# Performance work log

Hardware: AMD Instinct MI355X
Metric: run time of the kernel (lower is better)

Reference implementation:

```python
import jax, jax.numpy as jnp
import numpy as np

INPUT_SIZE, HIDDEN_SIZE, MEMORY_SIZE, SEQ_LEN, THETA = 512, 1024, 256, 4096, 4096.0
BATCH = 8


def _expm(M):
    # scaling-and-squaring Taylor expm (float64), replaces scipy cont2discrete's expm
    nrm = np.linalg.norm(M, 1)
    s = max(0, int(np.ceil(np.log2(max(nrm, 1.0)))) + 4)
    A = M / (2.0 ** s)
    E = np.eye(M.shape[0])
    T = np.eye(M.shape[0])
    for k in range(1, 24):
        T = T @ A / k
        E = E + T
    for _ in range(s):
        E = E @ E
    return E


def _lmu_H():
    # continuous-time Legendre state-space matrices
    Q = np.arange(MEMORY_SIZE, dtype=np.float64).reshape(-1, 1)
    R = (2.0 * Q + 1.0) / THETA
    i, j = np.meshgrid(Q.ravel(), Q.ravel(), indexing="ij")
    A = R * np.where(i < j, -1.0, (-1.0) ** (i - j + 1))
    B = R * (-1.0) ** Q
    # zero-order-hold discretization with dt=1: expm([[A,B],[0,0]])
    aug = np.zeros((MEMORY_SIZE + 1, MEMORY_SIZE + 1))
    aug[:MEMORY_SIZE, :MEMORY_SIZE] = A
    aug[:MEMORY_SIZE, MEMORY_SIZE:] = B
    Md = _expm(aug)
    Ad = Md[:MEMORY_SIZE, :MEMORY_SIZE].astype(np.float32)
    Bd = Md[:MEMORY_SIZE, MEMORY_SIZE:].astype(np.float32)
    # impulse response: H[:, t] = Ad^t @ Bd  (matches torch impulse() in float32)
    H = np.empty((MEMORY_SIZE, SEQ_LEN), dtype=np.float32)
    h = Bd[:, 0]
    for t in range(SEQ_LEN):
        H[:, t] = h
        h = Ad @ h
    return H


def setup_inputs():
    key = jax.random.key(0)
    k1, k2, k3, k4, k5 = jax.random.split(key, 5)
    x = jax.random.normal(k1, (BATCH, SEQ_LEN, INPUT_SIZE), jnp.float32)
    W_u_w = jax.random.normal(k2, (1, INPUT_SIZE), jnp.float32) / np.float32(np.sqrt(INPUT_SIZE))
    W_u_b = jax.random.normal(k3, (1,), jnp.float32) * 0.01
    W_h_w = jax.random.normal(k4, (HIDDEN_SIZE, MEMORY_SIZE + INPUT_SIZE), jnp.float32) / np.float32(np.sqrt(MEMORY_SIZE + INPUT_SIZE))
    W_h_b = jax.random.normal(k5, (HIDDEN_SIZE,), jnp.float32) * 0.01
    H = jnp.asarray(_lmu_H())
    return {"x": x, "W_u_w": W_u_w, "W_u_b": W_u_b, "W_h_w": W_h_w, "W_h_b": W_h_b, "H": H}


def reference(x, W_u_w, W_u_b, W_h_w, W_h_b, H):
    B, S, D = x.shape
    # u_t = relu(W_u x_t)  -> [B, S, 1]
    u = jax.nn.relu(jnp.einsum("bsd,od->bso", x, W_u_w) + W_u_b)
    # FFT long convolution of u with impulse response H (linear conv via 2S padding)
    fft_u = jnp.fft.rfft(u.transpose(0, 2, 1), n=2 * S, axis=-1)  # [B, 1, S+1]
    fft_H = jnp.fft.rfft(H, n=2 * S, axis=-1)                     # [M, S+1]
    m = jnp.fft.irfft(fft_u * fft_H[None], n=2 * S, axis=-1)[:, :, :S]  # [B, M, S]
    m = m.transpose(0, 2, 1)                                      # [B, S, M]
    # h_t = relu(W_h [m_t; x_t])
    h = jax.nn.relu(jnp.einsum("bsk,hk->bsh", jnp.concatenate([m, x], axis=-1), W_h_w) + W_h_b)
    return h, h[:, -1, :]
```

## Files before the change

kernel.cpp:

```cpp
#include <hip/hip_runtime.h>

typedef _Float16 half8 __attribute__((ext_vector_type(8)));
typedef float f32x4 __attribute__((ext_vector_type(4)));

#define SEQ   4096
#define DIN   512
#define HID   1024
#define KMEM  256
#define NB    8
#define KC    768
#define VP    4352
#define OUT_H_ELEMS 33554432ull

__device__ __forceinline__ void load_lds16(const void* g, void* l) {
  __builtin_amdgcn_global_load_lds(
      (const __attribute__((address_space(1))) unsigned int*)g,
      (__attribute__((address_space(3))) unsigned int*)l, 16, 0, 0);
}

__global__ __launch_bounds__(256) void prep_kernel(
    const float* __restrict__ Hf, const float* __restrict__ Wf,
    _Float16* __restrict__ Hh, _Float16* __restrict__ Wh,
    _Float16* __restrict__ v2)
{
  int tid = blockIdx.x * 256 + threadIdx.x;
  int stride = gridDim.x * 256;
  for (int i = tid; i < KMEM * SEQ; i += stride) Hh[i] = (_Float16)Hf[i];
  for (int i = tid; i < HID * KC;  i += stride) Wh[i] = (_Float16)Wf[i];
  for (int i = tid; i < NB * 8 * VP; i += stride) v2[i] = (_Float16)0.f;
}

__global__ __launch_bounds__(256) void u_kernel(
    const float* __restrict__ x, const float* __restrict__ Wu,
    const float* __restrict__ Wub,
    _Float16* __restrict__ xh, _Float16* __restrict__ v2)
{
  int w = threadIdx.x >> 6, lane = threadIdx.x & 63;
  int row = blockIdx.x * 4 + w;
  const float4* xr = (const float4*)(x + (size_t)row * DIN);
  const float4* wr = (const float4*)Wu;
  float4 a0 = xr[lane * 2], a1 = xr[lane * 2 + 1];
  float4 w0 = wr[lane * 2], w1 = wr[lane * 2 + 1];
  float dot = a0.x * w0.x + a0.y * w0.y + a0.z * w0.z + a0.w * w0.w
            + a1.x * w1.x + a1.y * w1.y + a1.z * w1.z + a1.w * w1.w;
  half8 hv;
  hv[0] = (_Float16)a0.x; hv[1] = (_Float16)a0.y;
  hv[2] = (_Float16)a0.z; hv[3] = (_Float16)a0.w;
  hv[4] = (_Float16)a1.x; hv[5] = (_Float16)a1.y;
  hv[6] = (_Float16)a1.z; hv[7] = (_Float16)a1.w;
  *((half8*)(xh + (size_t)row * DIN + lane * 8)) = hv;
  #pragma unroll
  for (int off = 32; off > 0; off >>= 1) dot += __shfl_xor(dot, off);
  float u = dot + Wub[0];
  u = u > 0.f ? u : 0.f;
  if (lane < 8) {
    int s = row & (SEQ - 1), b = row >> 12;
    v2[(size_t)b * 8 * VP + (size_t)lane * VP + (4095 - s + lane)] = (_Float16)u;
  }
}

__global__ __launch_bounds__(256) void conv_kernel(
    const _Float16* __restrict__ Hh, const _Float16* __restrict__ v2,
    _Float16* __restrict__ mh)
{
  __shared__ _Float16 Bs[128 * 32];
  __shared__ _Float16 Aw[8 * 168];
  int cb = blockIdx.x;
  int b = cb >> 1, kt = cb & 1;
  int by = blockIdx.y;
  int its = (by < 16) ? (31 - by) : (by - 16);
  int s0 = its * 128, k0 = kt * 128;
  int tid = threadIdx.x;
  int w = tid >> 6, lane = tid & 63;
  int wr = w >> 1, wc = w & 1;
  int lm = lane & 15, q = lane >> 4;
  const _Float16* v2b = v2 + (size_t)b * 8 * VP;
  int gbase0 = 3968 - s0;

  const _Float16* aoff[4];
  #pragma unroll
  for (int mi = 0; mi < 4; mi++) {
    int X = wr * 64 + mi * 16 + lm;
    int p = (X + 1) & 7;
    aoff[mi] = Aw + p * 168 + (127 - X + p) + q * 8;
  }
  const _Float16* boff[4];
  #pragma unroll
  for (int ni = 0; ni < 4; ni++)
    boff[ni] = Bs + (wc * 64 + ni * 16 + lm) * 32 + q * 8;

  int ap = tid / 21, aidx = tid - ap * 21;

  f32x4 acc[4][4] = {};
  int iters = 4 * (its + 1);
  for (int it = 0; it < iters; ++it) {
    int r0 = it * 32;
    __syncthreads();
    if (tid < 168)
      load_lds16(v2b + (size_t)ap * VP + gbase0 + r0 + aidx * 8, Aw + tid * 8);
    #pragma unroll
    for (int p2 = 0; p2 < 2; p2++) {
      int c = p2 * 256 + tid;
      int col = c >> 2, ch = c & 3;
      load_lds16(Hh + (size_t)(k0 + col) * SEQ + r0 + ch * 8, Bs + (size_t)c * 8);
    }
    __syncthreads();
    half8 af[4], bf[4];
    #pragma unroll
    for (int mi = 0; mi < 4; mi++) af[mi] = *((const half8*)(aoff[mi]));
    #pragma unroll
    for (int ni = 0; ni < 4; ni++) bf[ni] = *((const half8*)(boff[ni]));
    #pragma unroll
    for (int mi = 0; mi < 4; mi++)
      #pragma unroll
      for (int ni = 0; ni < 4; ni++)
        acc[mi][ni] = __builtin_amdgcn_mfma_f32_16x16x32_f16(af[mi], bf[ni], acc[mi][ni], 0, 0, 0);
  }
  size_t rowbase = (size_t)b * SEQ;
  #pragma unroll
  for (int mi = 0; mi < 4; mi++) {
    #pragma unroll
    for (int ni = 0; ni < 4; ni++) {
      int kout = k0 + wc * 64 + ni * 16 + lm;
      #pragma unroll
      for (int r = 0; r < 4; r++) {
        int sout = s0 + wr * 64 + mi * 16 + q * 4 + r;
        mh[(rowbase + sout) * KMEM + kout] = (_Float16)acc[mi][ni][r];
      }
    }
  }
}

__global__ __launch_bounds__(256) void h_kernel(
    const _Float16* __restrict__ mh, const _Float16* __restrict__ xh,
    const _Float16* __restrict__ Wh, const float* __restrict__ Whb,
    float* __restrict__ out)
{
  __shared__ _Float16 As[128 * 32];
  __shared__ _Float16 Bs[128 * 32];
  int nt = blockIdx.x, mt = blockIdx.y;
  int tid = threadIdx.x, w = tid >> 6, lane = tid & 63;
  int wr = w >> 1, wc = w & 1, lm = lane & 15, q = lane >> 4;

  f32x4 acc[4][4] = {};
  for (int it = 0; it < 24; ++it) {
    int kk = it * 32;
    __syncthreads();
    #pragma unroll
    for (int p2 = 0; p2 < 2; p2++) {
      int c = p2 * 256 + tid;
      int row = c >> 2, ch = c & 3;
      size_t rg = (size_t)mt * 128 + row;
      const _Float16* srcA = (kk < KMEM)
          ? (mh + rg * KMEM + kk + ch * 8)
          : (xh + rg * DIN + (kk - KMEM) + ch * 8);
      load_lds16(srcA, As + (size_t)c * 8);
      const _Float16* srcB = Wh + (size_t)(nt * 128 + row) * KC + kk + ch * 8;
      load_lds16(srcB, Bs + (size_t)c * 8);
    }
    __syncthreads();
    half8 af[4], bf[4];
    #pragma unroll
    for (int mi = 0; mi < 4; mi++)
      af[mi] = *((const half8*)(As + (wr * 64 + mi * 16 + lm) * 32 + q * 8));
    #pragma unroll
    for (int ni = 0; ni < 4; ni++)
      bf[ni] = *((const half8*)(Bs + (wc * 64 + ni * 16 + lm) * 32 + q * 8));
    #pragma unroll
    for (int mi = 0; mi < 4; mi++)
      #pragma unroll
      for (int ni = 0; ni < 4; ni++)
        acc[mi][ni] = __builtin_amdgcn_mfma_f32_16x16x32_f16(af[mi], bf[ni], acc[mi][ni], 0, 0, 0);
  }
  #pragma unroll
  for (int ni = 0; ni < 4; ni++) {
    int colg = nt * 128 + wc * 64 + ni * 16 + lm;
    float bias = Whb[colg];
    #pragma unroll
    for (int mi = 0; mi < 4; mi++) {
      #pragma unroll
      for (int r = 0; r < 4; r++) {
        int rowg = mt * 128 + wr * 64 + mi * 16 + q * 4 + r;
        float v = acc[mi][ni][r] + bias;
        v = v > 0.f ? v : 0.f;
        out[(size_t)rowg * HID + colg] = v;
        if ((rowg & (SEQ - 1)) == SEQ - 1)
          out[OUT_H_ELEMS + (size_t)(rowg >> 12) * HID + colg] = v;
      }
    }
  }
}

extern "C" void kernel_launch(void* const* d_in, const int* in_sizes, int n_in,
                              void* d_out, int out_size, void* d_ws, size_t ws_size,
                              hipStream_t stream) {
  const float* x   = (const float*)d_in[0];
  const float* Wu  = (const float*)d_in[1];
  const float* Wub = (const float*)d_in[2];
  const float* Whw = (const float*)d_in[3];
  const float* Whb = (const float*)d_in[4];
  const float* Hf  = (const float*)d_in[5];
  float* out = (float*)d_out;

  char* ws = (char*)d_ws;
  _Float16* Hh = (_Float16*)(ws);
  _Float16* Wh = (_Float16*)(ws + 2097152);
  _Float16* v2 = (_Float16*)(ws + 3670016);
  _Float16* xh = (_Float16*)(ws + 4227072);
  _Float16* mh = (_Float16*)(ws + 37781504);

  prep_kernel<<<dim3(1024), dim3(256), 0, stream>>>(Hf, Whw, Hh, Wh, v2);
  u_kernel<<<dim3(8192), dim3(256), 0, stream>>>(x, Wu, Wub, xh, v2);
  conv_kernel<<<dim3(16, 32), dim3(256), 0, stream>>>(Hh, v2, mh);
  h_kernel<<<dim3(8, 256), dim3(256), 0, stream>>>(mh, xh, Wh, Whb, out);
}
```

Baseline: 373.2 us.

## Double-buffer LDS tiles in conv and h GEMMs and remap h blocks across XCDs

```diff
diff --git a/kernel.cpp b/kernel.cpp
--- a/kernel.cpp
+++ b/kernel.cpp
@@ -63,8 +63,8 @@
     const _Float16* __restrict__ Hh, const _Float16* __restrict__ v2,
     _Float16* __restrict__ mh)
 {
-  __shared__ _Float16 Bs[128 * 32];
-  __shared__ _Float16 Aw[8 * 168];
+  __shared__ _Float16 Bs[2][128 * 32];
+  __shared__ _Float16 Aw[2][8 * 168];
   int cb = blockIdx.x;
   int b = cb >> 1, kt = cb & 1;
   int by = blockIdx.y;
@@ -77,39 +77,53 @@
   const _Float16* v2b = v2 + (size_t)b * 8 * VP;
   int gbase0 = 3968 - s0;
 
-  const _Float16* aoff[4];
+  int aoffs[4];
   #pragma unroll
   for (int mi = 0; mi < 4; mi++) {
     int X = wr * 64 + mi * 16 + lm;
     int p = (X + 1) & 7;
-    aoff[mi] = Aw + p * 168 + (127 - X + p) + q * 8;
-  }
-  const _Float16* boff[4];
+    aoffs[mi] = p * 168 + (127 - X + p) + q * 8;
+  }
+  int boffs[4];
   #pragma unroll
   for (int ni = 0; ni < 4; ni++)
-    boff[ni] = Bs + (wc * 64 + ni * 16 + lm) * 32 + q * 8;
+    boffs[ni] = (wc * 64 + ni * 16 + lm) * 32 + q * 8;
 
   int ap = tid / 21, aidx = tid - ap * 21;
 
   f32x4 acc[4][4] = {};
   int iters = 4 * (its + 1);
-  for (int it = 0; it < iters; ++it) {
-    int r0 = it * 32;
-    __syncthreads();
+
+  {
     if (tid < 168)
-      load_lds16(v2b + (size_t)ap * VP + gbase0 + r0 + aidx * 8, Aw + tid * 8);
+      load_lds16(v2b + (size_t)ap * VP + gbase0 + aidx * 8, Aw[0] + tid * 8);
     #pragma unroll
     for (int p2 = 0; p2 < 2; p2++) {
       int c = p2 * 256 + tid;
       int col = c >> 2, ch = c & 3;
-      load_lds16(Hh + (size_t)(k0 + col) * SEQ + r0 + ch * 8, Bs + (size_t)c * 8);
-    }
+      load_lds16(Hh + (size_t)(k0 + col) * SEQ + ch * 8, Bs[0] + (size_t)c * 8);
+    }
+  }
+
+  for (int it = 0; it < iters; ++it) {
+    int buf = it & 1;
     __syncthreads();
+    if (it + 1 < iters) {
+      int r0 = (it + 1) * 32;
+      if (tid < 168)
+        load_lds16(v2b + (size_t)ap * VP + gbase0 + r0 + aidx * 8, Aw[buf ^ 1] + tid * 8);
+      #pragma unroll
+      for (int p2 = 0; p2 < 2; p2++) {
+        int c = p2 * 256 + tid;
+        int col = c >> 2, ch = c & 3;
+        load_lds16(Hh + (size_t)(k0 + col) * SEQ + r0 + ch * 8, Bs[buf ^ 1] + (size_t)c * 8);
+      }
+    }
     half8 af[4], bf[4];
     #pragma unroll
-    for (int mi = 0; mi < 4; mi++) af[mi] = *((const half8*)(aoff[mi]));
-    #pragma unroll
-    for (int ni = 0; ni < 4; ni++) bf[ni] = *((const half8*)(boff[ni]));
+    for (int mi = 0; mi < 4; mi++) af[mi] = *((const half8*)(Aw[buf] + aoffs[mi]));
+    #pragma unroll
+    for (int ni = 0; ni < 4; ni++) bf[ni] = *((const half8*)(Bs[buf] + boffs[ni]));
     #pragma unroll
     for (int mi = 0; mi < 4; mi++)
       #pragma unroll
@@ -136,36 +150,52 @@
     const _Float16* __restrict__ Wh, const float* __restrict__ Whb,
     float* __restrict__ out)
 {
-  __shared__ _Float16 As[128 * 32];
-  __shared__ _Float16 Bs[128 * 32];
-  int nt = blockIdx.x, mt = blockIdx.y;
+  __shared__ _Float16 As[2][128 * 32];
+  __shared__ _Float16 Bs[2][128 * 32];
+  int id = blockIdx.y * 8 + blockIdx.x;
+  int xcd = id & 7;
+  int j = id >> 3;
+  int mt = (j >> 3) * 8 + xcd;
+  int nt = j & 7;
   int tid = threadIdx.x, w = tid >> 6, lane = tid & 63;
   int wr = w >> 1, wc = w & 1, lm = lane & 15, q = lane >> 4;
 
   f32x4 acc[4][4] = {};
-  for (int it = 0; it < 24; ++it) {
-    int kk = it * 32;
-    __syncthreads();
+  {
     #pragma unroll
     for (int p2 = 0; p2 < 2; p2++) {
       int c = p2 * 256 + tid;
       int row = c >> 2, ch = c & 3;
       size_t rg = (size_t)mt * 128 + row;
-      const _Float16* srcA = (kk < KMEM)
-          ? (mh + rg * KMEM + kk + ch * 8)
-          : (xh + rg * DIN + (kk - KMEM) + ch * 8);
-      load_lds16(srcA, As + (size_t)c * 8);
-      const _Float16* srcB = Wh + (size_t)(nt * 128 + row) * KC + kk + ch * 8;
-      load_lds16(srcB, Bs + (size_t)c * 8);
-    }
+      load_lds16(mh + rg * KMEM + ch * 8, As[0] + (size_t)c * 8);
+      load_lds16(Wh + (size_t)(nt * 128 + row) * KC + ch * 8, Bs[0] + (size_t)c * 8);
+    }
+  }
+  for (int it = 0; it < 24; ++it) {
+    int buf = it & 1;
     __syncthreads();
+    if (it + 1 < 24) {
+      int kk = (it + 1) * 32;
+      #pragma unroll
+      for (int p2 = 0; p2 < 2; p2++) {
+        int c = p2 * 256 + tid;
+        int row = c >> 2, ch = c & 3;
+        size_t rg = (size_t)mt * 128 + row;
+        const _Float16* srcA = (kk < KMEM)
+            ? (mh + rg * KMEM + kk + ch * 8)
+            : (xh + rg * DIN + (kk - KMEM) + ch * 8);
+        load_lds16(srcA, As[buf ^ 1] + (size_t)c * 8);
+        load_lds16(Wh + (size_t)(nt * 128 + row) * KC + kk + ch * 8,
+                   Bs[buf ^ 1] + (size_t)c * 8);
+      }
+    }
     half8 af[4], bf[4];
     #pragma unroll
     for (int mi = 0; mi < 4; mi++)
-      af[mi] = *((const half8*)(As + (wr * 64 + mi * 16 + lm) * 32 + q * 8));
+      af[mi] = *((const half8*)(As[buf] + (wr * 64 + mi * 16 + lm) * 32 + q * 8));
     #pragma unroll
     for (int ni = 0; ni < 4; ni++)
-      bf[ni] = *((const half8*)(Bs + (wc * 64 + ni * 16 + lm) * 32 + q * 8));
+      bf[ni] = *((const half8*)(Bs[buf] + (wc * 64 + ni * 16 + lm) * 32 + q * 8));
     #pragma unroll
     for (int mi = 0; mi < 4; mi++)
       #pragma unroll
```

New measurement: 345.4 us. 1.08x faster.
